# Kernel optimization log

Hardware: AMD Instinct MI355X
Metric: run time of the kernel (lower is better)

Reference implementation:

```python
import jax, jax.numpy as jnp
import numpy as np

B, NS, D, NE = 4096, 64, 256, 16  # walkers, determinant slots, d_model, electrons


def setup_inputs() -> dict:
    key = jax.random.key(0)
    k_y, k_up, k_dn, k_r = jax.random.split(key, 4)
    y = jax.random.normal(k_y, (B, NS, D), dtype=jnp.float32)
    # xavier_uniform over (d_model, Ne) fan axes
    limit = np.sqrt(6.0 / (D + NE)).astype(np.float32)
    M1_up_real = jax.random.uniform(k_up, (NS, D, NE), dtype=jnp.float32, minval=-limit, maxval=limit)
    M1_down_real = jax.random.uniform(k_dn, (NS, D, NE), dtype=jnp.float32, minval=-limit, maxval=limit)
    # R: Ne distinct orbital-row indices per walker in [0, 2*Ns)
    keys = jax.random.split(k_r, B)
    R = jax.vmap(lambda k: jax.random.permutation(k, 2 * NS)[:NE])(keys).astype(jnp.int32)
    return {"y": y, "M1_up_real": M1_up_real, "M1_down_real": M1_down_real, "R": R}


def reference(y, M1_up_real, M1_down_real, R):
    # orbitals: per-slot linear map of features -> Ne orbital values
    orb_up = jnp.einsum('bnd,nde->bne', y, M1_up_real)      # (B, Ns, Ne)
    orb_dn = jnp.einsum('bnd,nde->bne', y, M1_down_real)    # (B, Ns, Ne)
    orbitals = jnp.concatenate((orb_up, orb_dn), axis=1)     # (B, 2*Ns, Ne)
    # gather Ne rows per walker -> batched square matrices (B, Ne, Ne)
    A = jnp.take_along_axis(orbitals, R[:, :, None], axis=1)
    sign, logabsdet = jnp.linalg.slogdet(A)
    cdtype = jnp.complex64
    amp = logabsdet.astype(cdtype) + jnp.log(sign.astype(cdtype))
    return jnp.where(jnp.isnan(amp), -jnp.inf, amp)          # (B,) complex64
```

## Files before the change

kernel.cpp:

```cpp
#include <hip/hip_runtime.h>
#include <math.h>

#define BWALK 4096
#define NS 64
#define DD 256
#define NE 16
#define NSLOT 128
#define CHUNK 512
#define ROWBH 264

typedef __attribute__((ext_vector_type(4))) float f32x4;
typedef __attribute__((ext_vector_type(8))) short s16x8;

union Frag  { s16x8 v; unsigned u[4]; uint4 q; };

__device__ inline unsigned rne_bf16(float x) {
    unsigned u = __float_as_uint(x);
    return (u + 0x7fffu + ((u >> 16) & 1u)) >> 16;
}
__device__ inline float bf16_to_f(unsigned h) { return __uint_as_float(h << 16); }

__global__ __launch_bounds__(256) void orbitals_fused_kernel(
    const float* __restrict__ y,
    const float* __restrict__ Mup,
    const float* __restrict__ Mdn,
    const int* __restrict__ R,
    float* __restrict__ A)
{
    const int n   = blockIdx.x;
    const int b0  = blockIdx.y * CHUNK;
    const int tid = threadIdx.x;
    const int lane = tid & 63;
    const int wv   = tid >> 6;

    __shared__ uint4 sBH[8 * 64];
    __shared__ uint4 sBL[8 * 64];
    __shared__ __align__(16) unsigned char sY[4 * 2 * 16 * ROWBH];
    __shared__ int sCode[CHUNK];
    __shared__ int wsum[4];

    int m[2];
    int cnt = 0;
    #pragma unroll
    for (int q = 0; q < 2; ++q) {
        const int b = b0 + tid * 2 + q;
        const int4* rp = (const int4*)(R + (size_t)b * NE);
        int mi = -1;
        #pragma unroll
        for (int t4 = 0; t4 < 4; ++t4) {
            const int4 r4 = rp[t4];
            if (r4.x == n) mi = t4 * 4 + 0;
            if (r4.y == n) mi = t4 * 4 + 1;
            if (r4.z == n) mi = t4 * 4 + 2;
            if (r4.w == n) mi = t4 * 4 + 3;
        }
        m[q] = mi;
        cnt += (mi >= 0) ? 1 : 0;
    }

    int incl = cnt;
    #pragma unroll
    for (int off = 1; off < 64; off <<= 1) {
        const int x = __shfl_up(incl, off, 64);
        if (lane >= off) incl += x;
    }
    if (lane == 63) wsum[wv] = incl;

    {
        const float* Msrc = (n < NS ? Mup : Mdn) + (size_t)(n & (NS - 1)) * (DD * NE);
        #pragma unroll
        for (int pp = 0; pp < 2; ++pp) {
            const int p  = tid + pp * 256;
            const int kc = p >> 6;
            const int lt = p & 63;
            const int kg = lt >> 4;
            const int e  = lt & 15;
            unsigned h[8], l[8];
            #pragma unroll
            for (int j = 0; j < 8; ++j) {
                const float f = Msrc[(kc * 32 + kg * 8 + j) * 16 + e];
                const unsigned hh = rne_bf16(f);
                h[j] = hh;
                l[j] = rne_bf16(f - bf16_to_f(hh));
            }
            uint4 vh, vl;
            vh.x = h[0] | (h[1] << 16); vh.y = h[2] | (h[3] << 16);
            vh.z = h[4] | (h[5] << 16); vh.w = h[6] | (h[7] << 16);
            vl.x = l[0] | (l[1] << 16); vl.y = l[2] | (l[3] << 16);
            vl.z = l[4] | (l[5] << 16); vl.w = l[6] | (l[7] << 16);
            sBH[p] = vh;
            sBL[p] = vl;
        }
    }
    __syncthreads();

    int base = incl - cnt;
    #pragma unroll
    for (int w = 0; w < 3; ++w) if (w < wv) base += wsum[w];
    const int total = wsum[0] + wsum[1] + wsum[2] + wsum[3];
    {
        int p = base;
        #pragma unroll
        for (int q = 0; q < 2; ++q) {
            if (m[q] >= 0) {
                const int b = b0 + tid * 2 + q;
                sCode[p++] = (b << 4) | m[q];
            }
        }
    }
    __syncthreads();

    if (total == 0) return;

    const int e  = lane & 15;
    const int kg = lane >> 4;
    const int slot = n & (NS - 1);

    char* waveBase = (char*)sY + wv * (2 * 16 * ROWBH);
    char* hiBase = waveBase;
    char* loBase = waveBase + 16 * ROWBH;

    for (int g = wv * 16; g < total; g += 64) {
        const int gme = g + e;
        const int mycode = sCode[gme < total ? gme : (total - 1)];

        f32x4 acc0 = {0.f, 0.f, 0.f, 0.f};
        f32x4 acc1 = {0.f, 0.f, 0.f, 0.f};
        f32x4 acc2 = {0.f, 0.f, 0.f, 0.f};

        #pragma unroll
        for (int h = 0; h < 2; ++h) {
            f32x4 vv[8];
            #pragma unroll
            for (int rr = 0; rr < 8; ++rr) {
                const int idx = g + 2 * rr + (lane >> 5);
                const int code = sCode[idx < total ? idx : (total - 1)];
                const float* row = y + ((size_t)(code >> 4) * NS + slot) * DD;
                vv[rr] = *(const f32x4*)(row + h * 128 + (lane & 31) * 4);
            }
            #pragma unroll
            for (int rr = 0; rr < 8; ++rr) {
                unsigned hh[4], ll[4];
                #pragma unroll
                for (int j = 0; j < 4; ++j) {
                    const float f = vv[rr][j];
                    hh[j] = rne_bf16(f);
                    ll[j] = rne_bf16(f - bf16_to_f(hh[j]));
                }
                uint2 hw, lw;
                hw.x = hh[0] | (hh[1] << 16); hw.y = hh[2] | (hh[3] << 16);
                lw.x = ll[0] | (ll[1] << 16); lw.y = ll[2] | (ll[3] << 16);
                const int r = 2 * rr + (lane >> 5);
                *(uint2*)(hiBase + r * ROWBH + (lane & 31) * 8) = hw;
                *(uint2*)(loBase + r * ROWBH + (lane & 31) * 8) = lw;
            }

            #pragma unroll
            for (int kcl = 0; kcl < 4; ++kcl) {
                const int kc = h * 4 + kcl;
                Frag ahi, alo, bh, bl;
                ahi.q = *(const uint4*)(hiBase + e * ROWBH + kcl * 64 + kg * 16);
                alo.q = *(const uint4*)(loBase + e * ROWBH + kcl * 64 + kg * 16);
                bh.q = sBH[kc * 64 + lane];
                bl.q = sBL[kc * 64 + lane];
                acc0 = __builtin_amdgcn_mfma_f32_16x16x32_bf16(ahi.v, bh.v, acc0, 0, 0, 0);
                acc1 = __builtin_amdgcn_mfma_f32_16x16x32_bf16(ahi.v, bl.v, acc1, 0, 0, 0);
                acc2 = __builtin_amdgcn_mfma_f32_16x16x32_bf16(alo.v, bh.v, acc2, 0, 0, 0);
            }
        }
        const f32x4 acc = acc0 + (acc1 + acc2);

        #pragma unroll
        for (int r = 0; r < 4; ++r) {
            const int j = kg * 4 + r;
            const int jcode = __shfl(mycode, j, 16);
            if (g + j < total) A[(size_t)jcode * NE + e] = acc[r];
        }
    }
}

__global__ __launch_bounds__(256) void lu_det_kernel(
    const float* __restrict__ A, float* __restrict__ out, int mode)
{
    const int tid = threadIdx.x;
    const int w = blockIdx.x * 16 + (tid >> 4);
    const int lane = tid & 15;

    float a[NE];
    {
        const f32x4* p = (const f32x4*)(A + ((size_t)w * NE + lane) * NE);
        #pragma unroll
        for (int q = 0; q < 4; ++q) {
            const f32x4 vv = p[q];
            a[q * 4 + 0] = vv[0]; a[q * 4 + 1] = vv[1];
            a[q * 4 + 2] = vv[2]; a[q * 4 + 3] = vv[3];
        }
    }

    unsigned used = 0u;
    float logabs = 0.0f;
    int neg = 0;
    int perm[NE];

    #pragma unroll
    for (int k = 0; k < NE; ++k) {
        float v = ((used >> lane) & 1u) ? -1.0f : fabsf(a[k]);
        int bi = lane;
        #pragma unroll
        for (int off = 8; off > 0; off >>= 1) {
            const float ov = __shfl_xor(v, off, 16);
            const int   oi = __shfl_xor(bi, off, 16);
            if (ov > v || (ov == v && oi < bi)) { v = ov; bi = oi; }
        }
        const int p = bi;
        perm[k] = p;
        const float pivval = __shfl(a[k], p, 16);
        const bool active = (((used >> lane) & 1u) == 0u) && (lane != p);
        const float mlt = active ? (a[k] / pivval) : 0.0f;
        #pragma unroll
        for (int ee = k + 1; ee < NE; ++ee) {
            const float pe = __shfl(a[ee], p, 16);
            a[ee] = fmaf(-mlt, pe, a[ee]);
        }
        used |= (1u << p);
        logabs += logf(fabsf(pivval));
        neg ^= (pivval < 0.0f) ? 1 : 0;
    }

    int inv = 0;
    #pragma unroll
    for (int k1 = 0; k1 < NE; ++k1) {
        #pragma unroll
        for (int k2 = k1 + 1; k2 < NE; ++k2)
            inv ^= (perm[k1] > perm[k2]) ? 1 : 0;
    }
    neg ^= inv;

    if (lane == 0) {
        float re = logabs;
        float im = neg ? 3.14159274101257324f : 0.0f;
        if (__builtin_isnan(re)) { re = -INFINITY; im = 0.0f; }
        else if (re == -INFINITY) { im = 0.0f; }
        if (mode == 0) { out[2 * w] = re; out[2 * w + 1] = im; }
        else           { out[w] = re; }
    }
}

__global__ __launch_bounds__(256) void outputheaddet_kernel(
    const float* __restrict__ y,
    const float* __restrict__ Mup,
    const float* __restrict__ Mdn,
    const int* __restrict__ R,
    float* __restrict__ out,
    int mode)
{
    const int b = blockIdx.x;
    const int tid = threadIdx.x;

    __shared__ int   sR[NE];
    __shared__ float sYf[NE][DD];
    __shared__ float sA[NE][NE + 1];

    if (tid < NE) sR[tid] = R[b * NE + tid];
    __syncthreads();

    {
        const int i  = tid >> 4;
        const int d0 = (tid & 15) * 16;
        const int n    = sR[i];
        const int slot = n & (NS - 1);
        const float4* yp = reinterpret_cast<const float4*>(
            y + (((size_t)b * NS + slot) * DD + d0));
        float4 v0 = yp[0], v1 = yp[1], v2 = yp[2], v3 = yp[3];
        float4* dst = reinterpret_cast<float4*>(&sYf[i][d0]);
        dst[0] = v0; dst[1] = v1; dst[2] = v2; dst[3] = v3;
    }
    __syncthreads();

    {
        const int i = tid >> 4;
        const int e = tid & 15;
        const int n    = sR[i];
        const int slot = n & (NS - 1);
        const float* Mp = (n < NS ? Mup : Mdn) + (size_t)slot * (DD * NE) + e;
        float acc = 0.0f;
        #pragma unroll 8
        for (int d = 0; d < DD; ++d)
            acc = fmaf(sYf[i][d], Mp[(size_t)d * NE], acc);
        sA[i][e] = acc;
    }
    __syncthreads();

    if (tid >= NE) return;

    const int lane = tid;
    float a[NE];
    #pragma unroll
    for (int e = 0; e < NE; ++e) a[e] = sA[lane][e];

    unsigned used = 0u;
    float logabs = 0.0f;
    int neg = 0;
    int perm[NE];

    #pragma unroll
    for (int k = 0; k < NE; ++k) {
        float v = ((used >> lane) & 1u) ? -1.0f : fabsf(a[k]);
        int bi = lane;
        #pragma unroll
        for (int off = 8; off > 0; off >>= 1) {
            float ov = __shfl_xor(v, off, 16);
            int   oi = __shfl_xor(bi, off, 16);
            if (ov > v || (ov == v && oi < bi)) { v = ov; bi = oi; }
        }
        const int p = bi;
        perm[k] = p;
        const float pivval = __shfl(a[k], p, 16);
        const bool active = (((used >> lane) & 1u) == 0u) && (lane != p);
        const float mlt = active ? (a[k] / pivval) : 0.0f;
        #pragma unroll
        for (int e2 = k + 1; e2 < NE; ++e2) {
            const float pe = __shfl(a[e2], p, 16);
            a[e2] = fmaf(-mlt, pe, a[e2]);
        }
        used |= (1u << p);
        logabs += logf(fabsf(pivval));
        neg ^= (pivval < 0.0f) ? 1 : 0;
    }

    int inv = 0;
    #pragma unroll
    for (int k1 = 0; k1 < NE; ++k1) {
        #pragma unroll
        for (int k2 = k1 + 1; k2 < NE; ++k2)
            inv ^= (perm[k1] > perm[k2]) ? 1 : 0;
    }
    neg ^= inv;

    if (lane == 0) {
        float re = logabs;
        float im = neg ? 3.14159274101257324f : 0.0f;
        if (__builtin_isnan(re)) { re = -INFINITY; im = 0.0f; }
        else if (re == -INFINITY) { im = 0.0f; }
        if (mode == 0) { out[2 * b] = re; out[2 * b + 1] = im; }
        else           { out[b] = re; }
    }
}

extern "C" void kernel_launch(void* const* d_in, const int* in_sizes, int n_in,
                              void* d_out, int out_size, void* d_ws, size_t ws_size,
                              hipStream_t stream) {
    const float* y   = (const float*)d_in[0];
    const float* Mup = (const float*)d_in[1];
    const float* Mdn = (const float*)d_in[2];
    const int*   R   = (const int*)d_in[3];
    float* out = (float*)d_out;

    const int mode = (out_size >= 2 * BWALK) ? 0 : 1;
    const size_t needA = (size_t)BWALK * NE * NE * sizeof(float);

    if (ws_size >= needA) {
        float* A = (float*)d_ws;
        hipLaunchKernelGGL(orbitals_fused_kernel, dim3(NSLOT, BWALK / CHUNK), dim3(256), 0, stream,
                           y, Mup, Mdn, R, A);
        hipLaunchKernelGGL(lu_det_kernel, dim3(BWALK / 16), dim3(256), 0, stream,
                           A, out, mode);
    } else {
        hipLaunchKernelGGL(outputheaddet_kernel, dim3(BWALK), dim3(256), 0, stream,
                           y, Mup, Mdn, R, out, mode);
    }
}
```

Measured before the change: 41.71 us.

## Build global per-slot bin lists in a separate pass before orbital MFMA

Replaces the per-block scan of R (each block scanned 512 walkers for its slot) with a dedicated binning kernel that uses shared and global atomics to build a list of (walker, electron) codes per orbital slot. The orbital kernel then reads its slot's list directly and splits it across 4 blocks, using lane shuffles instead of shared-memory code lookups. This removes the redundant R reads repeated across 128 slots and the prefix-scan overhead. In exchange it adds a memset and an extra kernel launch, and silently drops entries if any bin exceeds 1024.

```diff
diff --git a/kernel.cpp b/kernel.cpp
--- a/kernel.cpp
+++ b/kernel.cpp
@@ -6,7 +6,7 @@
 #define DD 256
 #define NE 16
 #define NSLOT 128
-#define CHUNK 512
+#define MAXBIN 1024
 #define ROWBH 264
 
 typedef __attribute__((ext_vector_type(4))) float f32x4;
@@ -20,51 +20,59 @@
 }
 __device__ inline float bf16_to_f(unsigned h) { return __uint_as_float(h << 16); }
 
-__global__ __launch_bounds__(256) void orbitals_fused_kernel(
+__global__ __launch_bounds__(256) void binbuild2_kernel(
+    const int* __restrict__ R, int* __restrict__ gcount, int* __restrict__ binlist)
+{
+    __shared__ int lcount[NSLOT];
+    __shared__ int lbase[NSLOT];
+    __shared__ int lrun[NSLOT];
+    const int tid = threadIdx.x;
+    if (tid < NSLOT) { lcount[tid] = 0; lrun[tid] = 0; }
+    __syncthreads();
+
+    const int b = blockIdx.x * 256 + tid;
+    int nn[NE];
+    {
+        const int4* rp = (const int4*)(R + (size_t)b * NE);
+        const int4 r0 = rp[0], r1 = rp[1], r2 = rp[2], r3 = rp[3];
+        nn[0]=r0.x; nn[1]=r0.y; nn[2]=r0.z; nn[3]=r0.w;
+        nn[4]=r1.x; nn[5]=r1.y; nn[6]=r1.z; nn[7]=r1.w;
+        nn[8]=r2.x; nn[9]=r2.y; nn[10]=r2.z; nn[11]=r2.w;
+        nn[12]=r3.x; nn[13]=r3.y; nn[14]=r3.z; nn[15]=r3.w;
+    }
+    #pragma unroll
+    for (int i = 0; i < NE; ++i) atomicAdd(&lcount[nn[i]], 1);
+    __syncthreads();
+    if (tid < NSLOT) lbase[tid] = atomicAdd(&gcount[tid], lcount[tid]);
+    __syncthreads();
+    #pragma unroll
+    for (int i = 0; i < NE; ++i) {
+        const int r = atomicAdd(&lrun[nn[i]], 1);
+        const int pos = lbase[nn[i]] + r;
+        if (pos < MAXBIN) binlist[nn[i] * MAXBIN + pos] = (b << 4) | i;
+    }
+}
+
+__global__ __launch_bounds__(256) void orbitals2_kernel(
     const float* __restrict__ y,
     const float* __restrict__ Mup,
     const float* __restrict__ Mdn,
-    const int* __restrict__ R,
+    const int* __restrict__ gcount,
+    const int* __restrict__ binlist,
     float* __restrict__ A)
 {
     const int n   = blockIdx.x;
-    const int b0  = blockIdx.y * CHUNK;
+    const int c   = blockIdx.y;
     const int tid = threadIdx.x;
     const int lane = tid & 63;
     const int wv   = tid >> 6;
 
+    const int cnt = gcount[n];
+    if (cnt == 0) return;
+
     __shared__ uint4 sBH[8 * 64];
     __shared__ uint4 sBL[8 * 64];
     __shared__ __align__(16) unsigned char sY[4 * 2 * 16 * ROWBH];
-    __shared__ int sCode[CHUNK];
-    __shared__ int wsum[4];
-
-    int m[2];
-    int cnt = 0;
-    #pragma unroll
-    for (int q = 0; q < 2; ++q) {
-        const int b = b0 + tid * 2 + q;
-        const int4* rp = (const int4*)(R + (size_t)b * NE);
-        int mi = -1;
-        #pragma unroll
-        for (int t4 = 0; t4 < 4; ++t4) {
-            const int4 r4 = rp[t4];
-            if (r4.x == n) mi = t4 * 4 + 0;
-            if (r4.y == n) mi = t4 * 4 + 1;
-            if (r4.z == n) mi = t4 * 4 + 2;
-            if (r4.w == n) mi = t4 * 4 + 3;
-        }
-        m[q] = mi;
-        cnt += (mi >= 0) ? 1 : 0;
-    }
-
-    int incl = cnt;
-    #pragma unroll
-    for (int off = 1; off < 64; off <<= 1) {
-        const int x = __shfl_up(incl, off, 64);
-        if (lane >= off) incl += x;
-    }
-    if (lane == 63) wsum[wv] = incl;
 
     {
         const float* Msrc = (n < NS ? Mup : Mdn) + (size_t)(n & (NS - 1)) * (DD * NE);
@@ -94,35 +102,19 @@
     }
     __syncthreads();
 
-    int base = incl - cnt;
-    #pragma unroll
-    for (int w = 0; w < 3; ++w) if (w < wv) base += wsum[w];
-    const int total = wsum[0] + wsum[1] + wsum[2] + wsum[3];
-    {
-        int p = base;
-        #pragma unroll
-        for (int q = 0; q < 2; ++q) {
-            if (m[q] >= 0) {
-                const int b = b0 + tid * 2 + q;
-                sCode[p++] = (b << 4) | m[q];
-            }
-        }
-    }
-    __syncthreads();
-
-    if (total == 0) return;
-
     const int e  = lane & 15;
     const int kg = lane >> 4;
     const int slot = n & (NS - 1);
+    const int* blist = binlist + n * MAXBIN;
 
     char* waveBase = (char*)sY + wv * (2 * 16 * ROWBH);
     char* hiBase = waveBase;
     char* loBase = waveBase + 16 * ROWBH;
 
-    for (int g = wv * 16; g < total; g += 64) {
-        const int gme = g + e;
-        const int mycode = sCode[gme < total ? gme : (total - 1)];
+    for (int t = c * 4 + wv; t * 16 < cnt; t += 16) {
+        const int g = t * 16;
+        const int ge = g + e;
+        const int myc = blist[ge < cnt ? ge : (cnt - 1)];
 
         f32x4 acc0 = {0.f, 0.f, 0.f, 0.f};
         f32x4 acc1 = {0.f, 0.f, 0.f, 0.f};
@@ -133,8 +125,8 @@
             f32x4 vv[8];
             #pragma unroll
             for (int rr = 0; rr < 8; ++rr) {
-                const int idx = g + 2 * rr + (lane >> 5);
-                const int code = sCode[idx < total ? idx : (total - 1)];
+                const int rloc = 2 * rr + (lane >> 5);
+                const int code = __shfl(myc, rloc, 16);
                 const float* row = y + ((size_t)(code >> 4) * NS + slot) * DD;
                 vv[rr] = *(const f32x4*)(row + h * 128 + (lane & 31) * 4);
             }
@@ -173,8 +165,8 @@
         #pragma unroll
         for (int r = 0; r < 4; ++r) {
             const int j = kg * 4 + r;
-            const int jcode = __shfl(mycode, j, 16);
-            if (g + j < total) A[(size_t)jcode * NE + e] = acc[r];
+            const int jcode = __shfl(myc, j, 16);
+            if (g + j < cnt) A[(size_t)jcode * NE + e] = acc[r];
         }
     }
 }
@@ -357,12 +349,21 @@
     float* out = (float*)d_out;
 
     const int mode = (out_size >= 2 * BWALK) ? 0 : 1;
-    const size_t needA = (size_t)BWALK * NE * NE * sizeof(float);
-
-    if (ws_size >= needA) {
-        float* A = (float*)d_ws;
-        hipLaunchKernelGGL(orbitals_fused_kernel, dim3(NSLOT, BWALK / CHUNK), dim3(256), 0, stream,
-                           y, Mup, Mdn, R, A);
+
+    const size_t off_list = 1024;
+    const size_t off_A    = off_list + (size_t)NSLOT * MAXBIN * sizeof(int);
+    const size_t need     = off_A + (size_t)BWALK * NE * NE * sizeof(float);
+
+    if (ws_size >= need) {
+        int*   gcount  = (int*)d_ws;
+        int*   binlist = (int*)((char*)d_ws + off_list);
+        float* A       = (float*)((char*)d_ws + off_A);
+
+        hipMemsetAsync(gcount, 0, NSLOT * sizeof(int), stream);
+        hipLaunchKernelGGL(binbuild2_kernel, dim3(BWALK / 256), dim3(256), 0, stream,
+                           R, gcount, binlist);
+        hipLaunchKernelGGL(orbitals2_kernel, dim3(NSLOT, 4), dim3(256), 0, stream,
+                           y, Mup, Mdn, gcount, binlist, A);
         hipLaunchKernelGGL(lu_det_kernel, dim3(BWALK / 16), dim3(256), 0, stream,
                            A, out, mode);
     } else {
```

Measured after the change: 43.92 us. 5.3% more time.

## Use one wavefront per walker in LU with readlane pivot search and batched logs

Applied to the files above, without the earlier changes.

The LU determinant kernel now maps one walker to each 64-lane wavefront instead of four walkers per wave. Only 16 of the lanes do useful work and the other 48 duplicate it. This lets pivot search and row broadcasts use scalar readlane instead of shuffles: pivot selection packs |a| with the lane index into a single sortable key and reduces it through a readlane tree. The permutation sign is counted incrementally with popcount instead of an O(n^2) inversion pass, and pivots are multiplied in groups of four so only four fast __logf calls are needed instead of sixteen logf. The trade-offs are a quarter of the lane utilization, a four-times larger grid, possible overflow or underflow in the partial products, and a pivot tie-break that drops the low mantissa bits.

```diff
diff --git a/kernel.cpp b/kernel.cpp
--- a/kernel.cpp
+++ b/kernel.cpp
@@ -183,60 +183,67 @@
     const float* __restrict__ A, float* __restrict__ out, int mode)
 {
     const int tid = threadIdx.x;
-    const int w = blockIdx.x * 16 + (tid >> 4);
+    const int w = blockIdx.x * 4 + (tid >> 6);
     const int lane = tid & 15;
 
     float a[NE];
     {
-        const f32x4* p = (const f32x4*)(A + ((size_t)w * NE + lane) * NE);
+        const f32x4* p4 = (const f32x4*)(A + ((size_t)w * NE + lane) * NE);
         #pragma unroll
         for (int q = 0; q < 4; ++q) {
-            const f32x4 vv = p[q];
+            const f32x4 vv = p4[q];
             a[q * 4 + 0] = vv[0]; a[q * 4 + 1] = vv[1];
             a[q * 4 + 2] = vv[2]; a[q * 4 + 3] = vv[3];
         }
     }
 
     unsigned used = 0u;
+    int inv = 0;
+    int neg = 0;
+    float prods[4] = {1.0f, 1.0f, 1.0f, 1.0f};
+
+    #pragma unroll
+    for (int k = 0; k < NE; ++k) {
+        const unsigned bits = __float_as_uint(fabsf(a[k]));
+        const unsigned key = ((used >> lane) & 1u) ? 0u
+                            : ((bits & ~0xFu) | (15u - (unsigned)lane));
+        unsigned kk[16];
+        #pragma unroll
+        for (int r = 0; r < 16; ++r)
+            kk[r] = (unsigned)__builtin_amdgcn_readlane((int)key, r);
+        #pragma unroll
+        for (int s = 8; s > 0; s >>= 1) {
+            #pragma unroll
+            for (int r = 0; r < s; ++r) kk[r] = kk[r] > kk[r + s] ? kk[r] : kk[r + s];
+        }
+        const int p = 15 - (int)(kk[0] & 0xFu);
+
+        const bool active = (((used >> lane) & 1u) == 0u) && (lane != p);
+        inv += __popc((~used) & ((1u << p) - 1u));
+        used |= (1u << p);
+
+        const float pivval = __uint_as_float(
+            (unsigned)__builtin_amdgcn_readlane((int)__float_as_uint(a[k]), p));
+        prods[k >> 2] *= pivval;
+        const float mlt = active ? (a[k] / pivval) : 0.0f;
+
+        #pragma unroll
+        for (int ee = k + 1; ee < NE; ++ee) {
+            const float pe = __uint_as_float(
+                (unsigned)__builtin_amdgcn_readlane((int)__float_as_uint(a[ee]), p));
+            a[ee] = fmaf(-mlt, pe, a[ee]);
+        }
+    }
+
     float logabs = 0.0f;
-    int neg = 0;
-    int perm[NE];
-
-    #pragma unroll
-    for (int k = 0; k < NE; ++k) {
-        float v = ((used >> lane) & 1u) ? -1.0f : fabsf(a[k]);
-        int bi = lane;
-        #pragma unroll
-        for (int off = 8; off > 0; off >>= 1) {
-            const float ov = __shfl_xor(v, off, 16);
-            const int   oi = __shfl_xor(bi, off, 16);
-            if (ov > v || (ov == v && oi < bi)) { v = ov; bi = oi; }
-        }
-        const int p = bi;
-        perm[k] = p;
-        const float pivval = __shfl(a[k], p, 16);
-        const bool active = (((used >> lane) & 1u) == 0u) && (lane != p);
-        const float mlt = active ? (a[k] / pivval) : 0.0f;
-        #pragma unroll
-        for (int ee = k + 1; ee < NE; ++ee) {
-            const float pe = __shfl(a[ee], p, 16);
-            a[ee] = fmaf(-mlt, pe, a[ee]);
-        }
-        used |= (1u << p);
-        logabs += logf(fabsf(pivval));
-        neg ^= (pivval < 0.0f) ? 1 : 0;
-    }
-
-    int inv = 0;
-    #pragma unroll
-    for (int k1 = 0; k1 < NE; ++k1) {
-        #pragma unroll
-        for (int k2 = k1 + 1; k2 < NE; ++k2)
-            inv ^= (perm[k1] > perm[k2]) ? 1 : 0;
-    }
-    neg ^= inv;
-
-    if (lane == 0) {
+    #pragma unroll
+    for (int g = 0; g < 4; ++g) {
+        logabs += __logf(fabsf(prods[g]));
+        neg ^= (prods[g] < 0.0f) ? 1 : 0;
+    }
+    neg ^= (inv & 1);
+
+    if ((tid & 63) == 0) {
         float re = logabs;
         float im = neg ? 3.14159274101257324f : 0.0f;
         if (__builtin_isnan(re)) { re = -INFINITY; im = 0.0f; }
@@ -363,7 +370,7 @@
         float* A = (float*)d_ws;
         hipLaunchKernelGGL(orbitals_fused_kernel, dim3(NSLOT, BWALK / CHUNK), dim3(256), 0, stream,
                            y, Mup, Mdn, R, A);
-        hipLaunchKernelGGL(lu_det_kernel, dim3(BWALK / 16), dim3(256), 0, stream,
+        hipLaunchKernelGGL(lu_det_kernel, dim3(BWALK / 4), dim3(256), 0, stream,
                            A, out, mode);
     } else {
         hipLaunchKernelGGL(outputheaddet_kernel, dim3(BWALK), dim3(256), 0, stream,
```

After: 41.18 us. No clear change (-1.3%).
